# Kernel tuning notes

Measured on AMD Instinct MI355X. Metric: run time of the kernel, lower is better.

## Reference

```python
import jax, jax.numpy as jnp
import numpy as np

G = 7          # grid_size
A = 2          # anchors_per_cell
C = 3          # num_classes
L_COORD, L_OBJ, L_NOOBJ, L_CLS = 5.0, 1.0, 0.5, 2.0


def setup_inputs() -> dict:
    key = jax.random.key(0)
    k0, k1, k2, k3, k4 = jax.random.split(key, 5)
    B, M = 32768, 20
    predictions = jax.random.normal(k0, (B, G, G, A, 5 + C), dtype=jnp.float32)
    xy1 = jax.random.uniform(k1, (B, M, 2), dtype=jnp.float32) * 0.8
    wh = jax.random.uniform(k2, (B, M, 2), dtype=jnp.float32) * 0.19 + 0.01
    target_boxes = jnp.concatenate([xy1, xy1 + wh], axis=-1)  # valid x1<x2, y1<y2
    target_labels = jax.random.randint(k3, (B, M), 0, C, dtype=jnp.int32)
    num_objs = jax.random.randint(k4, (B,), 0, M + 1, dtype=jnp.int32)
    anchors = jnp.array([[0.971, 1.7338], [3.4579, 5.1653]], dtype=jnp.float32)
    class_weights = jnp.array([1.0, 4.9, 4.8], dtype=jnp.float32)
    return dict(predictions=predictions, target_boxes=target_boxes,
                target_labels=target_labels, num_objs=num_objs,
                anchors=anchors, class_weights=class_weights)


def assign_targets(target_boxes, target_labels, num_objs, anchors, B):
    """Vectorized scatter-based replacement of the nested python assignment loop."""
    M = target_boxes.shape[1]
    x1, y1, x2, y2 = [target_boxes[..., i] for i in range(4)]  # (B,M)
    cx, cy = (x1 + x2) * 0.5, (y1 + y2) * 0.5
    w, h = x2 - x1, y2 - y1
    valid = (w > 0) & (h > 0) & (jnp.arange(M)[None, :] < num_objs[:, None])
    gi = jnp.clip(jnp.floor(cy * G).astype(jnp.int32), 0, G - 1)
    gj = jnp.clip(jnp.floor(cx * G).astype(jnp.int32), 0, G - 1)
    wg, hg = w * G, h * G
    # anchor matching IoU (width/height only), (B,M,A)
    inter = jnp.minimum(wg[..., None], anchors[:, 0]) * jnp.minimum(hg[..., None], anchors[:, 1])
    union = (wg * hg)[..., None] + anchors[:, 0] * anchors[:, 1] - inter
    best_a = jnp.argmax(inter / (union + 1e-6), axis=-1).astype(jnp.int32)  # first max = torch loop tie-break
    aw = anchors[best_a, 0]
    ah = anchors[best_a, 1]
    tx = cx * G - gj.astype(jnp.float32)
    ty = cy * G - gi.astype(jnp.float32)
    tw = jnp.log(jnp.clip(wg, 0.01, None) / (aw + 1e-6))
    th = jnp.log(jnp.clip(hg, 0.01, None) / (ah + 1e-6))
    tvals = jnp.stack([tx, ty, tw, th], axis=-1)  # (B,M,4)
    N = B * G * G * A
    bidx = jnp.arange(B, dtype=jnp.int32)[:, None]
    flat = ((bidx * G + gi) * G + gj) * A + best_a  # (B,M)
    flat = jnp.where(valid, flat, N)                # invalid -> dropped by scatter
    idx = flat.ravel()
    obj_mask = jnp.zeros((N,), jnp.float32).at[idx].set(1.0, mode='drop')
    target_bbox = jnp.zeros((N, 4), jnp.float32).at[idx].set(tvals.reshape(-1, 4), mode='drop')
    target_cls = jnp.zeros((N,), jnp.int32).at[idx].set(target_labels.ravel(), mode='drop')
    shape = (B, G, G, A)
    return obj_mask.reshape(shape), target_bbox.reshape(shape + (4,)), target_cls.reshape(shape)


def reference(predictions, target_boxes, target_labels, num_objs, anchors, class_weights):
    B = predictions.shape[0]
    pred_obj = predictions[..., 0]
    pred_bbox = predictions[..., 1:5]
    pred_cls = predictions[..., 5:]
    m, target_bbox, target_cls = assign_targets(target_boxes, target_labels, num_objs, anchors, B)
    sp = jax.nn.softplus
    # BCE-with-logits: target is 1 on obj cells, 0 on noobj cells
    loss_obj = jnp.sum(m * sp(-pred_obj))
    loss_noobj = jnp.sum((1.0 - m) * sp(pred_obj))
    # smooth L1 (beta=1), summed over obj cells
    d = pred_bbox - target_bbox
    ad = jnp.abs(d)
    sl1 = jnp.where(ad < 1.0, 0.5 * d * d, ad - 0.5)
    loss_bbox = jnp.sum(m[..., None] * sl1)
    # weighted cross entropy on obj cells
    logZ = jax.nn.logsumexpimport if False else jax.scipy.special.logsumexp(pred_cls, axis=-1)
    logit_t = jnp.take_along_axis(pred_cls, target_cls[..., None], axis=-1)[..., 0]
    loss_cls = jnp.sum(m * class_weights[target_cls] * (logZ - logit_t))
    num_pos = jnp.maximum(jnp.sum(m), 1.0)
    total = (L_COORD * loss_bbox + L_OBJ * loss_obj + L_NOOBJ * loss_noobj + L_CLS * loss_cls) / num_pos
    return total
```

## Files before the change

### kernel.cpp

```cpp
#include <hip/hip_runtime.h>


namespace {
constexpr int kG = 7;
constexpr int kA = 2;
constexpr int kM = 20;
constexpr int kCells = kG * kG * kA;
constexpr int kCh = 8;
constexpr int kNB = 32;
constexpr int kBlock = 448;
constexpr int kTgt = kNB * kM;
constexpr int kIters = (kNB * kCells) / kBlock;
}

__device__ __forceinline__ float softplus_fast(float x) {
    return fmaxf(x, 0.0f) + __logf(1.0f + __expf(-fabsf(x)));
}

__global__ __launch_bounds__(kBlock) void det_loss_main(
    const float* __restrict__ preds,
    const float* __restrict__ tboxes,
    const int* __restrict__ tlabels,
    const int* __restrict__ nobjs,
    const float* __restrict__ anchors,
    const float* __restrict__ cweights,
    float* __restrict__ partial,
    int B)
{
    __shared__ float4 s_tv[kTgt];
    __shared__ short  s_cell[kTgt];
    __shared__ int    s_pos[kTgt];
    __shared__ int    s_nobj[kNB];
    __shared__ int    s_npos;
    __shared__ float  s_red[kBlock / 64][4];

    const int tid = threadIdx.x;
    const int b0 = blockIdx.x * kNB;

    if (tid < kNB) {
        const int b = b0 + tid;
        s_nobj[tid] = (b < B) ? nobjs[b] : 0;
    }
    if (tid == 0) s_npos = 0;
    __syncthreads();

    const float a00 = anchors[0], a01 = anchors[1];
    const float a10 = anchors[2], a11 = anchors[3];

    for (int j = tid; j < kTgt; j += kBlock) {
        const int bl = j / kM;
        const int m  = j - bl * kM;
        short cell = -1;
        float4 tv = make_float4(0.f, 0.f, 0.f, 0.f);
        if (b0 + bl < B) {
            const float4 box = ((const float4*)tboxes)[(size_t)b0 * kM + j];
            const float x1 = box.x, y1 = box.y, x2 = box.z, y2 = box.w;
            const float cx = (x1 + x2) * 0.5f, cy = (y1 + y2) * 0.5f;
            const float w = x2 - x1, h = y2 - y1;
            if (w > 0.f && h > 0.f && m < s_nobj[bl]) {
                const int gi = min(max((int)floorf(cy * (float)kG), 0), kG - 1);
                const int gj = min(max((int)floorf(cx * (float)kG), 0), kG - 1);
                const float wg = w * (float)kG, hg = h * (float)kG;
                const float i0 = fminf(wg, a00) * fminf(hg, a01);
                const float u0 = wg * hg + a00 * a01 - i0;
                const float r0 = i0 / (u0 + 1e-6f);
                const float i1 = fminf(wg, a10) * fminf(hg, a11);
                const float u1 = wg * hg + a10 * a11 - i1;
                const float r1 = i1 / (u1 + 1e-6f);
                const int a = (r1 > r0) ? 1 : 0;
                const float aw = a ? a10 : a00;
                const float ah = a ? a11 : a01;
                tv.x = cx * (float)kG - (float)gj;
                tv.y = cy * (float)kG - (float)gi;
                tv.z = __logf(fmaxf(wg, 0.01f) / (aw + 1e-6f));
                tv.w = __logf(fmaxf(hg, 0.01f) / (ah + 1e-6f));
                cell = (short)(bl * kCells + (gi * kG + gj) * kA + a);
            }
        }
        s_cell[j] = cell;
        s_tv[j] = tv;
    }
    __syncthreads();

    for (int j = tid; j < kTgt; j += kBlock) {
        const short c = s_cell[j];
        if (c >= 0) {
            const int bl = j / kM;
            const int m  = j - bl * kM;
            bool win = true;
            for (int m2 = m + 1; m2 < kM; ++m2) {
                if (s_cell[bl * kM + m2] == c) { win = false; break; }
            }
            if (win) {
                const int idx = atomicAdd(&s_npos, 1);
                s_pos[idx] = (j << 16) | (int)c;
            }
        }
    }
    __syncthreads();

    float accO = 0.f, accN = 0.f, accB = 0.f, accC = 0.f;
    const float* __restrict__ pblk = preds + (size_t)b0 * kCells * kCh;
    if (b0 + kNB <= B) {
        #pragma unroll
        for (int k = 0; k < kIters; ++k) {
            const float po = pblk[(size_t)(tid + k * kBlock) * kCh];
            accN += softplus_fast(po);
        }
    } else {
        const int ncell = (B - b0) * kCells;
        for (int i = tid; i < ncell; i += kBlock)
            accN += softplus_fast(pblk[(size_t)i * kCh]);
    }

    const int np = s_npos;
    const float cw0 = cweights[0], cw1 = cweights[1], cw2 = cweights[2];
    for (int t = tid; t < np; t += kBlock) {
        const int pk = s_pos[t];
        const int j  = pk >> 16;
        const int ci = pk & 0xFFFF;
        const float4* pc = (const float4*)(pblk + (size_t)ci * kCh);
        const float4 p0 = pc[0];
        const float4 p1 = pc[1];
        const float spp = softplus_fast(p0.x);
        accN -= spp;
        accO += spp - p0.x;
        const float4 tv = s_tv[j];
        float d, ad;
        d = p0.y - tv.x; ad = fabsf(d); accB += (ad < 1.f) ? 0.5f * d * d : ad - 0.5f;
        d = p0.z - tv.y; ad = fabsf(d); accB += (ad < 1.f) ? 0.5f * d * d : ad - 0.5f;
        d = p0.w - tv.z; ad = fabsf(d); accB += (ad < 1.f) ? 0.5f * d * d : ad - 0.5f;
        d = p1.x - tv.w; ad = fabsf(d); accB += (ad < 1.f) ? 0.5f * d * d : ad - 0.5f;
        const int lab = tlabels[(size_t)b0 * kM + j];
        const float c0 = p1.y, c1 = p1.z, c2 = p1.w;
        const float mx = fmaxf(c0, fmaxf(c1, c2));
        const float lse = mx + __logf(__expf(c0 - mx) + __expf(c1 - mx) + __expf(c2 - mx));
        const float logit = (lab == 0) ? c0 : ((lab == 1) ? c1 : c2);
        const float cwv   = (lab == 0) ? cw0 : ((lab == 1) ? cw1 : cw2);
        accC += cwv * (lse - logit);
    }

    float vals[4] = {accO, accN, accB, accC};
    #pragma unroll
    for (int k = 0; k < 4; ++k) {
        float v = vals[k];
        #pragma unroll
        for (int off = 32; off > 0; off >>= 1) v += __shfl_down(v, off, 64);
        vals[k] = v;
    }
    const int wave = tid >> 6;
    const int lane = tid & 63;
    if (lane == 0) {
        #pragma unroll
        for (int k = 0; k < 4; ++k) s_red[wave][k] = vals[k];
    }
    __syncthreads();
    if (tid == 0) {
        const int nb = gridDim.x;
        #pragma unroll
        for (int k = 0; k < 4; ++k) {
            float t = 0.f;
            #pragma unroll
            for (int w = 0; w < kBlock / 64; ++w) t += s_red[w][k];
            partial[(size_t)k * nb + blockIdx.x] = t;
        }
        partial[(size_t)4 * nb + blockIdx.x] = (float)np;
    }
}

__global__ __launch_bounds__(256) void det_loss_reduce(
    const float* __restrict__ partial, int nblocks, float* __restrict__ out)
{
    __shared__ float s_red[4][5];
    const int tid = threadIdx.x;
    float v[5] = {0.f, 0.f, 0.f, 0.f, 0.f};
    for (int i = tid; i < nblocks; i += 256) {
        #pragma unroll
        for (int k = 0; k < 5; ++k) v[k] += partial[(size_t)k * nblocks + i];
    }
    #pragma unroll
    for (int k = 0; k < 5; ++k) {
        float x = v[k];
        #pragma unroll
        for (int off = 32; off > 0; off >>= 1) x += __shfl_down(x, off, 64);
        v[k] = x;
    }
    const int wave = tid >> 6;
    const int lane = tid & 63;
    if (lane == 0) {
        #pragma unroll
        for (int k = 0; k < 5; ++k) s_red[wave][k] = v[k];
    }
    __syncthreads();
    if (tid == 0) {
        float t[5];
        #pragma unroll
        for (int k = 0; k < 5; ++k) {
            float s = 0.f;
            #pragma unroll
            for (int w = 0; w < 4; ++w) s += s_red[w][k];
            t[k] = s;
        }
        const float npv = fmaxf(t[4], 1.0f);
        out[0] = (5.0f * t[2] + 1.0f * t[0] + 0.5f * t[1] + 2.0f * t[3]) / npv;
    }
}

extern "C" void kernel_launch(void* const* d_in, const int* in_sizes, int n_in,
                              void* d_out, int out_size, void* d_ws, size_t ws_size,
                              hipStream_t stream) {
    const float* preds    = (const float*)d_in[0];
    const float* tboxes   = (const float*)d_in[1];
    const int*   tlabels  = (const int*)d_in[2];
    const int*   nobjs    = (const int*)d_in[3];
    const float* anchors  = (const float*)d_in[4];
    const float* cweights = (const float*)d_in[5];
    float* out = (float*)d_out;
    float* partial = (float*)d_ws;

    const int B = in_sizes[0] / (kCells * kCh);
    const int blocks = (B + kNB - 1) / kNB;

    det_loss_main<<<blocks, kBlock, 0, stream>>>(
        preds, tboxes, tlabels, nobjs, anchors, cweights, partial, B);
    det_loss_reduce<<<1, 256, 0, stream>>>(partial, blocks, out);
}
```

Baseline: 178.1 us.

## Replace sparse positive-cell gather with dense per-cell table and full-row loads

Drops the atomic-compacted list of positive cells. Each cell now looks up a shared-memory table, indexed by cell, that holds its winning target index. Every thread loads the full 8-float prediction row as two float4s and computes all loss terms, masked by whether the cell is positive. This removes the second divergent gather pass and the shared atomics, and turns the strided scalar objectness loads into contiguous vector loads. In exchange, bbox and class math (exp/log) now runs for every cell instead of only the positive ones, and shared-memory use grows.

Result: no change. 181.0 us (+1.6%).

```diff
diff --git a/kernel.cpp b/kernel.cpp
--- a/kernel.cpp
+++ b/kernel.cpp
@@ -10,7 +10,8 @@
 constexpr int kNB = 32;
 constexpr int kBlock = 448;
 constexpr int kTgt = kNB * kM;
-constexpr int kIters = (kNB * kCells) / kBlock;
+constexpr int kCellsBlk = kNB * kCells;
+constexpr int kIters = kCellsBlk / kBlock;
 }
 
 __device__ __forceinline__ float softplus_fast(float x) {
@@ -27,11 +28,12 @@
     float* __restrict__ partial,
     int B)
 {
-    __shared__ float4 s_tv[kTgt];
+    __shared__ float4 s_tv[kTgt + 1];
+    __shared__ float  s_cw[kTgt + 1];
+    __shared__ int    s_lab[kTgt + 1];
     __shared__ short  s_cell[kTgt];
-    __shared__ int    s_pos[kTgt];
+    __shared__ short  s_table[kCellsBlk];
     __shared__ int    s_nobj[kNB];
-    __shared__ int    s_npos;
     __shared__ float  s_red[kBlock / 64][4];
 
     const int tid = threadIdx.x;
@@ -41,7 +43,13 @@
         const int b = b0 + tid;
         s_nobj[tid] = (b < B) ? nobjs[b] : 0;
     }
-    if (tid == 0) s_npos = 0;
+    if (tid == 0) {
+        s_tv[kTgt] = make_float4(0.f, 0.f, 0.f, 0.f);
+        s_cw[kTgt] = 0.f;
+        s_lab[kTgt] = 0;
+    }
+    #pragma unroll
+    for (int k = 0; k < kIters; ++k) s_table[tid + k * kBlock] = -1;
     __syncthreads();
 
     const float a00 = anchors[0], a01 = anchors[1];
@@ -52,6 +60,8 @@
         const int m  = j - bl * kM;
         short cell = -1;
         float4 tv = make_float4(0.f, 0.f, 0.f, 0.f);
+        float cwv = 0.f;
+        int lab = 0;
         if (b0 + bl < B) {
             const float4 box = ((const float4*)tboxes)[(size_t)b0 * kM + j];
             const float x1 = box.x, y1 = box.y, x2 = box.z, y2 = box.w;
@@ -75,10 +85,14 @@
                 tv.z = __logf(fmaxf(wg, 0.01f) / (aw + 1e-6f));
                 tv.w = __logf(fmaxf(hg, 0.01f) / (ah + 1e-6f));
                 cell = (short)(bl * kCells + (gi * kG + gj) * kA + a);
+                lab = tlabels[(size_t)b0 * kM + j];
+                cwv = cweights[lab];
             }
         }
         s_cell[j] = cell;
         s_tv[j] = tv;
+        s_cw[j] = cwv;
+        s_lab[j] = lab;
     }
     __syncthreads();
 
@@ -91,56 +105,82 @@
             for (int m2 = m + 1; m2 < kM; ++m2) {
                 if (s_cell[bl * kM + m2] == c) { win = false; break; }
             }
-            if (win) {
-                const int idx = atomicAdd(&s_npos, 1);
-                s_pos[idx] = (j << 16) | (int)c;
-            }
+            if (win) s_table[c] = (short)j;
         }
     }
     __syncthreads();
 
     float accO = 0.f, accN = 0.f, accB = 0.f, accC = 0.f;
-    const float* __restrict__ pblk = preds + (size_t)b0 * kCells * kCh;
+    int npos = 0;
+    const float cw0 = cweights[0];  (void)cw0;
+    const float4* __restrict__ p4 = (const float4*)preds + (size_t)b0 * kCells * 2;
+
     if (b0 + kNB <= B) {
         #pragma unroll
         for (int k = 0; k < kIters; ++k) {
-            const float po = pblk[(size_t)(tid + k * kBlock) * kCh];
-            accN += softplus_fast(po);
+            const int i = tid + k * kBlock;
+            const float4 p0 = p4[2 * i];
+            const float4 p1 = p4[2 * i + 1];
+            const int j = s_table[i];
+            const bool pos = (j >= 0);
+            const int jj = pos ? j : kTgt;
+            const float m = pos ? 1.f : 0.f;
+            const float4 tv = s_tv[jj];
+            const float cwv = s_cw[jj];
+            const int lab = s_lab[jj];
+
+            const float po = p0.x;
+            const float spo = softplus_fast(po);
+            accN += spo - m * spo;
+            accO += m * (spo - po);
+
+            float d, ad, sb;
+            d = p0.y - tv.x; ad = fabsf(d); sb  = (ad < 1.f) ? 0.5f * d * d : ad - 0.5f;
+            d = p0.z - tv.y; ad = fabsf(d); sb += (ad < 1.f) ? 0.5f * d * d : ad - 0.5f;
+            d = p0.w - tv.z; ad = fabsf(d); sb += (ad < 1.f) ? 0.5f * d * d : ad - 0.5f;
+            d = p1.x - tv.w; ad = fabsf(d); sb += (ad < 1.f) ? 0.5f * d * d : ad - 0.5f;
+            accB += m * sb;
+
+            const float c0 = p1.y, c1 = p1.z, c2 = p1.w;
+            const float mx = fmaxf(c0, fmaxf(c1, c2));
+            const float lse = mx + __logf(__expf(c0 - mx) + __expf(c1 - mx) + __expf(c2 - mx));
+            const float logit = (lab == 0) ? c0 : ((lab == 1) ? c1 : c2);
+            accC += m * cwv * (lse - logit);
+            npos += pos ? 1 : 0;
         }
     } else {
         const int ncell = (B - b0) * kCells;
-        for (int i = tid; i < ncell; i += kBlock)
-            accN += softplus_fast(pblk[(size_t)i * kCh]);
-    }
-
-    const int np = s_npos;
-    const float cw0 = cweights[0], cw1 = cweights[1], cw2 = cweights[2];
-    for (int t = tid; t < np; t += kBlock) {
-        const int pk = s_pos[t];
-        const int j  = pk >> 16;
-        const int ci = pk & 0xFFFF;
-        const float4* pc = (const float4*)(pblk + (size_t)ci * kCh);
-        const float4 p0 = pc[0];
-        const float4 p1 = pc[1];
-        const float spp = softplus_fast(p0.x);
-        accN -= spp;
-        accO += spp - p0.x;
-        const float4 tv = s_tv[j];
-        float d, ad;
-        d = p0.y - tv.x; ad = fabsf(d); accB += (ad < 1.f) ? 0.5f * d * d : ad - 0.5f;
-        d = p0.z - tv.y; ad = fabsf(d); accB += (ad < 1.f) ? 0.5f * d * d : ad - 0.5f;
-        d = p0.w - tv.z; ad = fabsf(d); accB += (ad < 1.f) ? 0.5f * d * d : ad - 0.5f;
-        d = p1.x - tv.w; ad = fabsf(d); accB += (ad < 1.f) ? 0.5f * d * d : ad - 0.5f;
-        const int lab = tlabels[(size_t)b0 * kM + j];
-        const float c0 = p1.y, c1 = p1.z, c2 = p1.w;
-        const float mx = fmaxf(c0, fmaxf(c1, c2));
-        const float lse = mx + __logf(__expf(c0 - mx) + __expf(c1 - mx) + __expf(c2 - mx));
-        const float logit = (lab == 0) ? c0 : ((lab == 1) ? c1 : c2);
-        const float cwv   = (lab == 0) ? cw0 : ((lab == 1) ? cw1 : cw2);
-        accC += cwv * (lse - logit);
+        for (int i = tid; i < ncell; i += kBlock) {
+            const float4 p0 = p4[2 * i];
+            const float4 p1 = p4[2 * i + 1];
+            const int j = s_table[i];
+            const bool pos = (j >= 0);
+            const int jj = pos ? j : kTgt;
+            const float m = pos ? 1.f : 0.f;
+            const float4 tv = s_tv[jj];
+            const float cwv = s_cw[jj];
+            const int lab = s_lab[jj];
+            const float po = p0.x;
+            const float spo = softplus_fast(po);
+            accN += spo - m * spo;
+            accO += m * (spo - po);
+            float d, ad, sb;
+            d = p0.y - tv.x; ad = fabsf(d); sb  = (ad < 1.f) ? 0.5f * d * d : ad - 0.5f;
+            d = p0.z - tv.y; ad = fabsf(d); sb += (ad < 1.f) ? 0.5f * d * d : ad - 0.5f;
+            d = p0.w - tv.z; ad = fabsf(d); sb += (ad < 1.f) ? 0.5f * d * d : ad - 0.5f;
+            d = p1.x - tv.w; ad = fabsf(d); sb += (ad < 1.f) ? 0.5f * d * d : ad - 0.5f;
+            accB += m * sb;
+            const float c0 = p1.y, c1 = p1.z, c2 = p1.w;
+            const float mx = fmaxf(c0, fmaxf(c1, c2));
+            const float lse = mx + __logf(__expf(c0 - mx) + __expf(c1 - mx) + __expf(c2 - mx));
+            const float logit = (lab == 0) ? c0 : ((lab == 1) ? c1 : c2);
+            accC += m * cwv * (lse - logit);
+            npos += pos ? 1 : 0;
+        }
     }
 
     float vals[4] = {accO, accN, accB, accC};
+    float npf = (float)npos;
     #pragma unroll
     for (int k = 0; k < 4; ++k) {
         float v = vals[k];
@@ -148,11 +188,16 @@
         for (int off = 32; off > 0; off >>= 1) v += __shfl_down(v, off, 64);
         vals[k] = v;
     }
+    #pragma unroll
+    for (int off = 32; off > 0; off >>= 1) npf += __shfl_down(npf, off, 64);
+
+    __shared__ float s_np[kBlock / 64];
     const int wave = tid >> 6;
     const int lane = tid & 63;
     if (lane == 0) {
         #pragma unroll
         for (int k = 0; k < 4; ++k) s_red[wave][k] = vals[k];
+        s_np[wave] = npf;
     }
     __syncthreads();
     if (tid == 0) {
@@ -164,7 +209,10 @@
             for (int w = 0; w < kBlock / 64; ++w) t += s_red[w][k];
             partial[(size_t)k * nb + blockIdx.x] = t;
         }
-        partial[(size_t)4 * nb + blockIdx.x] = (float)np;
+        float tn = 0.f;
+        #pragma unroll
+        for (int w = 0; w < kBlock / 64; ++w) tn += s_np[w];
+        partial[(size_t)4 * nb + blockIdx.x] = tn;
     }
 }
 
```
